# Kernel tuning notes

Hardware: AMD Instinct MI355X
Metric: run time of the kernel (lower is better)

The kernel has to match this reference:

```python
import jax, jax.numpy as jnp
import numpy as np

B, T, NB = 8192, 18, 6
EH, DH = 256, 256
NIN = NB + 1  # encoder GRU input: bits + feedback scalar


def gru_cell(x, h, Wih, Whh, bih, bhh):
    # PyTorch GRU cell: gates ordered (r, z, n)
    gi = x @ Wih.T + bih
    gh = h @ Whh.T + bhh
    ir, iz, inn = jnp.split(gi, 3, axis=-1)
    hr, hz, hn = jnp.split(gh, 3, axis=-1)
    r = jax.nn.sigmoid(ir + hr)
    z = jax.nn.sigmoid(iz + hz)
    n = jnp.tanh(inn + r * hn)
    return (1.0 - z) * n + z * h


def run_gru_dir(seq, Wih, Whh, bih, bhh, reverse):
    # seq: [T, B, D] -> hidden outputs [T, B, H] (aligned to original time order)
    Bn, H = seq.shape[1], Whh.shape[1]
    def step(h, x):
        h2 = gru_cell(x, h, Wih, Whh, bih, bhh)
        return h2, h2
    _, outs = jax.lax.scan(step, jnp.zeros((Bn, H), seq.dtype), seq, reverse=reverse)
    return outs


def setup_inputs() -> dict:
    key = jax.random.key(0)
    ks = jax.random.split(key, 40)
    def w(k, shape, fan):
        s = 1.0 / np.sqrt(fan)
        return jax.random.uniform(k, shape, jnp.float32, -s, s)
    inp = {}
    inp['b'] = (jax.random.uniform(ks[0], (B, NB)) < 0.5).astype(jnp.float32)
    inp['noise1'] = jax.random.normal(ks[1], (B, T, 1), jnp.float32)
    inp['noise2'] = jax.random.normal(ks[2], (B, T, 1), jnp.float32)
    # encoder GRU (2 layers, unidirectional)
    inp['enc_Wih0'] = w(ks[3], (3 * EH, NIN), EH); inp['enc_Whh0'] = w(ks[4], (3 * EH, EH), EH)
    inp['enc_bih0'] = w(ks[5], (3 * EH,), EH);     inp['enc_bhh0'] = w(ks[6], (3 * EH,), EH)
    inp['enc_Wih1'] = w(ks[7], (3 * EH, EH), EH);  inp['enc_Whh1'] = w(ks[8], (3 * EH, EH), EH)
    inp['enc_bih1'] = w(ks[9], (3 * EH,), EH);     inp['enc_bhh1'] = w(ks[10], (3 * EH,), EH)
    inp['enc_lin_W'] = w(ks[11], (1, EH), EH);     inp['enc_lin_b'] = w(ks[12], (1,), EH)
    inp['weight_power'] = jnp.ones((T,), jnp.float32)
    # decoder GRU (2 layers, bidirectional)
    inp['dec_Wih0f'] = w(ks[13], (3 * DH, 1), DH);      inp['dec_Whh0f'] = w(ks[14], (3 * DH, DH), DH)
    inp['dec_bih0f'] = w(ks[15], (3 * DH,), DH);        inp['dec_bhh0f'] = w(ks[16], (3 * DH,), DH)
    inp['dec_Wih0b'] = w(ks[17], (3 * DH, 1), DH);      inp['dec_Whh0b'] = w(ks[18], (3 * DH, DH), DH)
    inp['dec_bih0b'] = w(ks[19], (3 * DH,), DH);        inp['dec_bhh0b'] = w(ks[20], (3 * DH,), DH)
    inp['dec_Wih1f'] = w(ks[21], (3 * DH, 2 * DH), DH); inp['dec_Whh1f'] = w(ks[22], (3 * DH, DH), DH)
    inp['dec_bih1f'] = w(ks[23], (3 * DH,), DH);        inp['dec_bhh1f'] = w(ks[24], (3 * DH,), DH)
    inp['dec_Wih1b'] = w(ks[25], (3 * DH, 2 * DH), DH); inp['dec_Whh1b'] = w(ks[26], (3 * DH, DH), DH)
    inp['dec_bih1b'] = w(ks[27], (3 * DH,), DH);        inp['dec_bhh1b'] = w(ks[28], (3 * DH,), DH)
    inp['dec_lin_W'] = w(ks[29], (NB, 2 * DH), 2 * DH); inp['dec_lin_b'] = w(ks[30], (NB,), 2 * DH)
    inp['weight_merge'] = jnp.ones((T, 2), jnp.float32)
    return inp


def reference(b, noise1, noise2,
              enc_Wih0, enc_Whh0, enc_bih0, enc_bhh0,
              enc_Wih1, enc_Whh1, enc_bih1, enc_bhh1,
              enc_lin_W, enc_lin_b, weight_power,
              dec_Wih0f, dec_Whh0f, dec_bih0f, dec_bhh0f,
              dec_Wih0b, dec_Whh0b, dec_bih0b, dec_bhh0b,
              dec_Wih1f, dec_Whh1f, dec_bih1f, dec_bhh1f,
              dec_Wih1b, dec_Whh1b, dec_bih1b, dec_bhh1b,
              dec_lin_W, dec_lin_b, weight_merge):
    Bn = b.shape[0]
    Tn = weight_power.shape[0]
    # power-normalized per-step weights: sqrt(w^2 * T / sum(w^2))
    wp = jnp.sqrt(weight_power ** 2 * Tn / jnp.sum(weight_power ** 2))

    def enc_step(carry, xs):
        h0, h1, z = carry
        n1, n2, wpt = xs
        inp = jnp.concatenate([b, z], axis=1)            # [B, NB+1]
        h0n = gru_cell(inp, h0, enc_Wih0, enc_Whh0, enc_bih0, enc_bhh0)
        h1n = gru_cell(h0n, h1, enc_Wih1, enc_Whh1, enc_bih1, enc_bhh1)
        xt = jnp.tanh(h1n @ enc_lin_W.T + enc_lin_b)     # [B, 1]
        xn = (xt - jnp.mean(xt)) / jnp.std(xt, ddof=1)   # training-mode batch norm over whole tensor
        y = xn * wpt + n1                                # received symbol
        return (h0n, h1n, y + n2), y                     # feedback z = y + noise2

    carry0 = (jnp.zeros((Bn, EH), b.dtype), jnp.zeros((Bn, EH), b.dtype), jnp.zeros((Bn, 1), b.dtype))
    xs = (jnp.swapaxes(noise1, 0, 1), jnp.swapaxes(noise2, 0, 1), wp)
    _, y_seq = jax.lax.scan(enc_step, carry0, xs)        # [T, B, 1]

    # bidirectional 2-layer decoder GRU over y
    o0f = run_gru_dir(y_seq, dec_Wih0f, dec_Whh0f, dec_bih0f, dec_bhh0f, False)
    o0b = run_gru_dir(y_seq, dec_Wih0b, dec_Whh0b, dec_bih0b, dec_bhh0b, True)
    s1 = jnp.concatenate([o0f, o0b], axis=-1)            # [T, B, 2*DH]
    o1f = run_gru_dir(s1, dec_Wih1f, dec_Whh1f, dec_bih1f, dec_bhh1f, False)
    o1b = run_gru_dir(s1, dec_Wih1b, dec_Whh1b, dec_bih1b, dec_bhh1b, True)

    # attention_type == 5: learned weighted merge over time, per direction
    wf = jnp.sqrt(weight_merge[:, 0] ** 2 * Tn / jnp.sum(weight_merge[:, 0] ** 2))
    wb = jnp.sqrt(weight_merge[:, 1] ** 2 * Tn / jnp.sum(weight_merge[:, 1] ** 2))
    rf = jnp.einsum('tbh,t->bh', o1f, wf)
    rb = jnp.einsum('tbh,t->bh', o1b, wb)
    rc = jnp.concatenate([rf, rb], axis=1)               # [B, 2*DH]
    out = jax.nn.sigmoid(rc @ dec_lin_W.T + dec_lin_b)   # bit_vector output -> sigmoid
    return out.reshape(Bn, -1, 1)
```

## Files before the change

kernel.cpp:

```cpp
#include <hip/hip_runtime.h>
#include <hip/hip_bf16.h>
#include <math.h>

#define BN_ 8192
#define TT 18
#define NBITS 6
#define HH 256
#define G3 768

typedef __hip_bfloat16 hbf16;
typedef __bf16 bf16x8 __attribute__((ext_vector_type(8)));
typedef float f32x4 __attribute__((ext_vector_type(4)));

__device__ inline float sigm(float x){ return 1.0f/(1.0f + __expf(-x)); }
__device__ inline float ftanh(float x){ float e = __expf(2.0f*x); return 1.0f - 2.0f/(e + 1.0f); }
__device__ inline float ldx(const void* p, int i, int bf){
    if(bf){ unsigned short u = ((const unsigned short*)p)[i]; return __uint_as_float(((unsigned)u)<<16); }
    return ((const float*)p)[i];
}
__device__ inline __bf16 f2b(float f){ hbf16 h = __float2bfloat16(f); return *reinterpret_cast<__bf16*>(&h); }
__device__ inline float b2f(__bf16 b){ unsigned short u = *reinterpret_cast<unsigned short*>(&b); return __uint_as_float(((unsigned)u)<<16); }
__device__ inline unsigned pack2(float a, float b){
    hbf16 lo = __float2bfloat16(a), hi = __float2bfloat16(b);
    return (unsigned)*(unsigned short*)&lo | ((unsigned)*(unsigned short*)&hi << 16);
}

__device__ __forceinline__ void gld_lds16(const void* g, void* l){
    __builtin_amdgcn_global_load_lds(
        (const __attribute__((address_space(1))) unsigned int*)g,
        (__attribute__((address_space(3))) unsigned int*)l, 16, 0, 0);
}

__global__ __launch_bounds__(256) void fillz(float* __restrict__ p, int n){
    for(int i = blockIdx.x*256 + threadIdx.x; i < n; i += gridDim.x*256) p[i] = 0.0f;
}
__global__ __launch_bounds__(256) void fillb(__bf16* __restrict__ p, int n){
    for(int i = blockIdx.x*256 + threadIdx.x; i < n; i += gridDim.x*256) p[i] = f2b(0.0f);
}

__global__ void prep_w(const void* wp, const void* wm, unsigned* flag,
                       float* wpn, float* wfn, float* wbn){
    if(threadIdx.x==0 && blockIdx.x==0){
        unsigned w0 = *(const unsigned*)wp;
        int bf = ((w0 >> 16) == (w0 & 0xFFFFu)) ? 1 : 0;
        flag[0] = (unsigned)bf;
        float s=0; for(int t=0;t<TT;t++){ float v=ldx(wp,t,bf); s += v*v; }
        for(int t=0;t<TT;t++){ float v=ldx(wp,t,bf); wpn[t] = sqrtf(v*v*TT/s); }
        float sf=0, sb=0;
        for(int t=0;t<TT;t++){ float f=ldx(wm,2*t,bf), b=ldx(wm,2*t+1,bf); sf += f*f; sb += b*b; }
        for(int t=0;t<TT;t++){
            float f=ldx(wm,2*t,bf), b=ldx(wm,2*t+1,bf);
            wfn[t] = sqrtf(f*f*TT/sf);
            wbn[t] = sqrtf(b*b*TT/sb);
        }
    }
}

struct CJ { const void* src; void* dst; int n; int K; int mode; };
struct CJs { CJ j[20]; };
__global__ __launch_bounds__(256) void conv_all(CJs J, const unsigned* __restrict__ flagp){
    const int bf = (int)*flagp;
    CJ c = J.j[blockIdx.y];
    for(int i = blockIdx.x*256 + threadIdx.x; i < c.n; i += gridDim.x*256){
        if(c.mode==1){
            int row = i / c.K, k = i - row*c.K;
            int g = row>>8, jj = row&255;
            int prow = ((jj>>4)*48) + g*16 + (jj&15);
            ((__bf16*)c.dst)[(size_t)prow*c.K + k] = f2b(ldx(c.src, i, bf));
        }else if(c.mode==2){
            int t = i >> 13, b = i & (BN_-1);
            ((float*)c.dst)[i] = ldx(c.src, b*TT + t, bf);
        }else{
            ((float*)c.dst)[i] = ldx(c.src, i, bf);
        }
    }
}

struct FQ {
    const __bf16* A1; const __bf16* W1; int K1;
    const __bf16* A2; const __bf16* W2; int K2;
    const float* bgi; const float* bgh;
    const __bf16* h; __bf16* hout;
    const void* bits; const void* wih0raw; const void* bih0raw;
    const void* linw; float* xt;
    const float* y; const void* wihraw; const void* bihraw; __bf16* s1t;
    float* racc; const float* wct;
};
struct FQ2 { FQ q[2]; };

template<int MODE>
__global__ __launch_bounds__((MODE>=2)?512:256, 4) void fused_step(FQ2 PP, const unsigned* __restrict__ flagp){
    const FQ P = PP.q[blockIdx.z];
    const int bf = (int)*flagp;
    constexpr int THREADS = (MODE>=2) ? 512 : 256;
    constexpr int BM   = (MODE<=1) ? 64 : 128;
    constexpr int WR   = (MODE>=2) ? 192 : 96;
    constexpr int JB   = WR/3;
    constexpr int NF   = BM/32;
    constexpr int ABYT = BM*64;
    constexpr int WBYT = WR*64;
    constexpr int BUFB = ABYT + WBYT;
    constexpr int TS   = JB + 1;
    __shared__ __align__(16) char smem[2*BUFB];
    __shared__ float zs[(MODE>=2)?384:192];
    __shared__ float sred[4], ssred[4];
    float*  T  = (float*)smem;
    const int tid = threadIdx.x;
    constexpr int JTBITS = (MODE>=2) ? 2 : 3;
    constexpr int MTS = (8192/BM)/8;
    const int mt = blockIdx.x*MTS + (blockIdx.y>>JTBITS);
    const int jt = blockIdx.y & ((1<<JTBITS)-1);
    const int m0 = mt*BM;
    const int n0 = jt*WR;
    const int lane = tid&63, wv = tid>>6;
    const int wvbase = tid & ~63;
    const int wrow = (MODE>=2) ? (wv>>2) : (wv>>1);
    const int wcol = wv & ((MODE>=2)?3:1);
    const int q = lane>>4, n15 = lane&15;

    constexpr int S1  = (MODE==1) ? 8 : (MODE==3 ? 16 : 0);
    constexpr int NST = S1 + 8;
    constexpr int KD1 = (MODE==3) ? 512 : 256;
    constexpr int KD2 = 256;
    const __bf16* pA1 = (S1>0) ? P.A1 + (size_t)m0*KD1 : (const __bf16*)nullptr;
    const __bf16* pW1 = (S1>0) ? P.W1 + (size_t)n0*KD1 : (const __bf16*)nullptr;
    const __bf16* pA2 = P.A2 + (size_t)m0*KD2;
    const __bf16* pW2 = P.W2 + (size_t)n0*KD2;
    const int r0 = tid>>2, sl0 = tid&3;
    const int q0 = sl0 ^ ((r0>>1)&3);
    const int rW1 = THREADS/4 + r0;
    const int qW1 = sl0 ^ ((rW1>>1)&3);

    auto STG = [&](int s){
        const __bf16* A; const __bf16* W; int K; int k0;
        if(s < S1){ A = pA1; W = pW1; K = KD1; k0 = s*32; }
        else      { A = pA2; W = pW2; K = KD2; k0 = (s-S1)*32; }
        char* buf = smem + (s&1)*BUFB;
        gld_lds16(A + (size_t)r0*K + k0 + q0*8, buf + (size_t)wvbase*16);
        gld_lds16(W + (size_t)r0*K + k0 + q0*8, buf + ABYT + (size_t)wvbase*16);
        if(tid < THREADS/2)
            gld_lds16(W + (size_t)rW1*K + k0 + qW1*8, buf + ABYT + (size_t)(THREADS+wvbase)*16);
    };

    STG(0);

    if(MODE==0){
        if(P.K1){
            const float lbv = ldx(P.linw, 0, bf);
            const float wt  = P.wct[0];
            const float* __restrict__ xr = P.xt;
            float s=0.0f, ss=0.0f;
            const float4* x4 = (const float4*)xr;
            for(int i=tid;i<BN_/4;i+=THREADS){
                float4 vv = x4[i];
                float a0=ftanh(vv.x+lbv), a1=ftanh(vv.y+lbv), a2=ftanh(vv.z+lbv), a3=ftanh(vv.w+lbv);
                s += a0+a1+a2+a3; ss += a0*a0+a1*a1+a2*a2+a3*a3;
            }
            #pragma unroll
            for(int o=32;o;o>>=1){ s += __shfl_xor(s,o); ss += __shfl_xor(ss,o); }
            if(lane==0){ sred[wv]=s; ssred[wv]=ss; }
            __syncthreads();
            float a = sred[0]+sred[1]+sred[2]+sred[3];
            float bq = ssred[0]+ssred[1]+ssred[2]+ssred[3];
            float mean = a/(float)BN_;
            float var = (bq - (float)BN_*mean*mean)/(float)(BN_-1);
            float rs = 1.0f/sqrtf(var);
            if(tid<BM){
                int row = m0 + tid;
                float v = ftanh(xr[row]+lbv);
                float yv = (v-mean)*rs*wt + P.y[row];
                zs[tid] = yv + ((const float*)P.wihraw)[row];
                if(jt==0){ ((float*)P.s1t)[row] = yv; P.racc[row] = 0.0f; }
            }
        }else{
            if(tid<BM) zs[tid] = 0.0f;
        }
        __syncthreads();
    }else{
        __syncthreads();
    }

    f32x4 accR[NF], accZ[NF], accN1[NF], accN2[NF];
    #pragma unroll
    for(int i=0;i<NF;i++){ accR[i]=(f32x4){0,0,0,0}; accZ[i]=(f32x4){0,0,0,0};
                           accN1[i]=(f32x4){0,0,0,0}; accN2[i]=(f32x4){0,0,0,0}; }

    #pragma unroll
    for(int s=0; s<NST; ++s){
        if(s+1 < NST) STG(s+1);
        const char* buf = smem + (s&1)*BUFB;
        const __bf16* Asb = (const __bf16*)buf;
        const __bf16* Wsb = (const __bf16*)(buf + ABYT);
        bf16x8 af[NF], bfr[3];
        #pragma unroll
        for(int i=0;i<NF;i++){
            int R = wrow*(BM/2)+i*16+n15;
            int col = q ^ ((R>>1)&3);
            af[i] = *(const bf16x8*)&Asb[R*32 + col*8];
        }
        #pragma unroll
        for(int g=0;g<3;g++){
            int RW = wcol*48+g*16+n15;
            int col = q ^ ((RW>>1)&3);
            bfr[g] = *(const bf16x8*)&Wsb[RW*32 + col*8];
        }
        #pragma unroll
        for(int i=0;i<NF;i++){
            accR[i] = __builtin_amdgcn_mfma_f32_16x16x32_bf16(af[i], bfr[0], accR[i], 0,0,0);
            accZ[i] = __builtin_amdgcn_mfma_f32_16x16x32_bf16(af[i], bfr[1], accZ[i], 0,0,0);
            if(s < S1) accN1[i] = __builtin_amdgcn_mfma_f32_16x16x32_bf16(af[i], bfr[2], accN1[i], 0,0,0);
            else       accN2[i] = __builtin_amdgcn_mfma_f32_16x16x32_bf16(af[i], bfr[2], accN2[i], 0,0,0);
        }
        __syncthreads();
    }

    const int jl = wcol*16 + n15;
    const int j  = jt*JB + jl;
    const float bghr = P.bgh[j], bghz = P.bgh[256+j], bghn = P.bgh[512+j];
    float bgir=0, bgiz=0, bgin=0;
    if(MODE==1 || MODE==3){ bgir = P.bgi[j]; bgiz = P.bgi[256+j]; bgin = P.bgi[512+j]; }
    float w0r[7], w0z[7], w0n[7];
    if(MODE==0){
        #pragma unroll
        for(int k=0;k<7;k++){
            w0r[k] = ldx(P.wih0raw, (j    )*7+k, bf);
            w0z[k] = ldx(P.wih0raw, (j+256)*7+k, bf);
            w0n[k] = ldx(P.wih0raw, (j+512)*7+k, bf);
        }
        bgir = ldx(P.bih0raw, j, bf); bgiz = ldx(P.bih0raw, j+256, bf); bgin = ldx(P.bih0raw, j+512, bf);
    }
    float wy_r=0, wy_z=0, wy_n=0;
    if(MODE==2){
        wy_r = ldx(P.wihraw, j, bf); wy_z = ldx(P.wihraw, j+256, bf); wy_n = ldx(P.wihraw, j+512, bf);
        bgir = ldx(P.bihraw, j, bf); bgiz = ldx(P.bihraw, j+256, bf); bgin = ldx(P.bihraw, j+512, bf);
    }
    const float linwj = (MODE==1) ? ldx(P.linw, j, bf) : 0.0f;

    #pragma unroll
    for(int i=0;i<NF;i++){
        const int rbl = wrow*(BM/2) + i*16 + q*4;
        float vred[4];
        #pragma unroll
        for(int r=0;r<4;r++){
            const int row_l = rbl + r;
            const int row = m0 + row_l;
            float gir, giz, gin;
            if(MODE==1 || MODE==3){
                gir = bgir; giz = bgiz; gin = accN1[i][r] + bgin;
            }else if(MODE==0){
                gir = bgir; giz = bgiz; gin = bgin;
                #pragma unroll
                for(int k=0;k<NBITS;k++){
                    float bv = ldx(P.bits, row*NBITS+k, bf);
                    gir += bv*w0r[k]; giz += bv*w0z[k]; gin += bv*w0n[k];
                }
                float zb = zs[row_l];
                gir += zb*w0r[6]; giz += zb*w0z[6]; gin += zb*w0n[6];
            }else{
                float yv = P.y[row];
                gir = yv*wy_r + bgir; giz = yv*wy_z + bgiz; gin = yv*wy_n + bgin;
            }
            float rr = sigm(gir + accR[i][r] + bghr);
            float zz = sigm(giz + accZ[i][r] + bghz);
            float nn = ftanh(gin + rr*(accN2[i][r] + bghn));
            float hold = b2f(P.h[(size_t)row*HH + j]);
            float hn = (1.0f - zz)*nn + zz*hold;
            T[row_l*TS + jl] = hn;
            if(MODE==1) vred[r] = hn*linwj;
        }
        if(MODE==1){
            #pragma unroll
            for(int r=0;r<4;r++){
                float v = vred[r];
                #pragma unroll
                for(int m=1;m<16;m<<=1) v += __shfl_xor(v, m);
                if(n15==0) atomicAdd(&P.xt[m0+rbl+r], v);
            }
        }
    }
    if(MODE==3 && tid<6*JB){
        int k = tid/JB, jj = tid - k*JB;
        zs[tid] = ldx(P.bits, k*512 + (int)blockIdx.z*256 + jt*JB + jj, bf);
    }
    __syncthreads();

    if constexpr(MODE<=1){
        const int rw2 = tid>>2, cw = tid&3;
        const int row_l = rw2;
        const int row = m0 + row_l;
        float v[8];
        #pragma unroll
        for(int u=0;u<8;u++) v[u] = T[row_l*TS + cw*8 + u];
        uint4 pkv = { pack2(v[0],v[1]), pack2(v[2],v[3]), pack2(v[4],v[5]), pack2(v[6],v[7]) };
        *(uint4*)&P.hout[(size_t)row*HH + jt*JB + cw*8] = pkv;
    }else{
        const int rw2 = tid>>3, cw = tid&7;
        #pragma unroll
        for(int pass=0; pass<2; pass++){
            const int row_l = pass*64 + rw2;
            const int row = m0 + row_l;
            float v[8];
            #pragma unroll
            for(int u=0;u<8;u++) v[u] = T[row_l*TS + cw*8 + u];
            uint4 pkv = { pack2(v[0],v[1]), pack2(v[2],v[3]), pack2(v[4],v[5]), pack2(v[6],v[7]) };
            *(uint4*)&P.hout[(size_t)row*HH + jt*JB + cw*8] = pkv;
            if(MODE==2) *(uint4*)&P.s1t[(size_t)row*512 + jt*JB + cw*8] = pkv;
        }
    }
    if(MODE==3){
        float* pp = P.xt + (size_t)(jt + 4*(int)blockIdx.z)*(BN_*NBITS);
        const float wct3 = P.wct[0];
        #pragma unroll
        for(int u=0;u<2;u++){
            int idx = tid + THREADS*u;
            if(idx < BM*NBITS){
                int row_l = idx/6, k = idx - row_l*6;
                float dot = 0.0f;
                #pragma unroll
                for(int jj=0;jj<JB;jj++) dot += T[row_l*TS+jj]*zs[k*JB+jj];
                size_t gi = (size_t)(m0+row_l)*NBITS + k;
                pp[gi] += wct3*dot;
            }
        }
    }
}

__global__ __launch_bounds__(1024) void stats_emit(float* __restrict__ xt, const void* __restrict__ lb,
        const float* __restrict__ wpn, int t, const float* __restrict__ n1t, const float* __restrict__ n2t,
        float* __restrict__ yseq, float* __restrict__ zf, const unsigned* __restrict__ flagp){
    const int bf = (int)*flagp;
    const float lbv = ldx(lb, 0, bf);
    int tid = threadIdx.x;
    float s=0.0f, ss=0.0f;
    for(int i=tid;i<BN_;i+=1024){ float v = ftanh(xt[i] + lbv); s += v; ss += v*v; }
    #pragma unroll
    for(int o=32;o;o>>=1){ s += __shfl_down(s,o); ss += __shfl_down(ss,o); }
    __shared__ float S[16], SS[16], stm[2];
    if((tid&63)==0){ S[tid>>6]=s; SS[tid>>6]=ss; }
    __syncthreads();
    if(tid==0){
        float a=0.0f, b=0.0f;
        for(int i=0;i<16;i++){ a+=S[i]; b+=SS[i]; }
        float mean = a/(float)BN_;
        float var = (b - (float)BN_*mean*mean)/(float)(BN_-1);
        stm[0]=mean; stm[1]=1.0f/sqrtf(var);
    }
    __syncthreads();
    const float mean=stm[0], rs=stm[1], wt=wpn[t];
    for(int i=tid;i<BN_;i+=1024){
        float v = ftanh(xt[i] + lbv);
        float y = (v-mean)*rs*wt + n1t[i];
        yseq[(size_t)t*BN_ + i] = y;
        zf[i] = y + n2t[i];
        xt[i] = 0.0f;
    }
}

__global__ __launch_bounds__(256) void out_head(const float* __restrict__ pp, const void* __restrict__ bias,
        void* __restrict__ out, const unsigned* __restrict__ flagp){
    const int bf = (int)*flagp;
    int i = blockIdx.x*256 + threadIdx.x;
    if(i >= BN_*NBITS) return;
    float s = 0.0f;
    #pragma unroll
    for(int k=0;k<8;k++) s += pp[(size_t)k*(BN_*NBITS) + i];
    int kk = i - (i/6)*6;
    float v = sigm(s + ldx(bias, kk, bf));
    if(bf) ((hbf16*)out)[i] = __float2bfloat16(v);
    else   ((float*)out)[i] = v;
}

extern "C" void kernel_launch(void* const* d_in, const int* in_sizes, int n_in,
                              void* d_out, int out_size, void* d_ws, size_t ws_size,
                              hipStream_t stream)
{
    (void)in_sizes; (void)n_in; (void)out_size;
    const void* bits  = d_in[0];
    const void* n1    = d_in[1];
    const void* n2    = d_in[2];
    const void* eWih0 = d_in[3];
    const void* eWhh0 = d_in[4];
    const void* ebih0 = d_in[5];
    const void* ebhh0 = d_in[6];
    const void* eWih1 = d_in[7];
    const void* eWhh1 = d_in[8];
    const void* ebih1 = d_in[9];
    const void* ebhh1 = d_in[10];
    const void* elinW = d_in[11];
    const void* elinb = d_in[12];
    const void* wpow  = d_in[13];
    const void* dWih0f= d_in[14];
    const void* dWhh0f= d_in[15];
    const void* dbih0f= d_in[16];
    const void* dbhh0f= d_in[17];
    const void* dWih0b= d_in[18];
    const void* dWhh0b= d_in[19];
    const void* dbih0b= d_in[20];
    const void* dbhh0b= d_in[21];
    const void* dWih1f= d_in[22];
    const void* dWhh1f= d_in[23];
    const void* dbih1f= d_in[24];
    const void* dbhh1f= d_in[25];
    const void* dWih1b= d_in[26];
    const void* dWhh1b= d_in[27];
    const void* dbih1b= d_in[28];
    const void* dbhh1b= d_in[29];
    const void* dlinW = d_in[30];
    const void* dlinb = d_in[31];
    const void* wmrg  = d_in[32];

    float* base = (float*)d_ws;
    size_t off = 0;
    auto alloc  = [&](size_t n){ float* p = base + off; off += (n + 63) & ~(size_t)63; return p; };
    auto allocb = [&](size_t n){ __bf16* p = (__bf16*)(base + off); off += ((n/2) + 63) & ~(size_t)63; return p; };
    unsigned* flag = (unsigned*)alloc(64);
    float* wpn = alloc(TT); float* wfn = alloc(TT); float* wbn = alloc(TT);
    const int WK = HH*G3;
    __bf16* WeHH0 = allocb(WK);  __bf16* WeIH1 = allocb(WK);  __bf16* WeHH1 = allocb(WK);
    __bf16* Wd0f  = allocb(WK);  __bf16* Wd0b  = allocb(WK);
    __bf16* Wd1fI = allocb(2*WK);__bf16* Wd1bI = allocb(2*WK);
    __bf16* Wd1fH = allocb(WK);  __bf16* Wd1bH = allocb(WK);
    float* BeHH0 = alloc(G3); float* BeIH1 = alloc(G3); float* BeHH1 = alloc(G3);
    float* Bd0f  = alloc(G3); float* Bd0b  = alloc(G3);
    float* Bd1fI = alloc(G3); float* Bd1bI = alloc(G3);
    float* Bd1fH = alloc(G3); float* Bd1bH = alloc(G3);
    const size_t NH = (size_t)BN_*HH;
    __bf16* X0 = allocb(NH);  __bf16* X1 = allocb(NH);
    __bf16* Y0 = allocb(NH);  __bf16* Y1 = allocb(NH);
    float* pout = alloc((size_t)8*BN_*NBITS);
    float* xtA = alloc(BN_);
    float* xtB = alloc(BN_);
    float* zf  = alloc(BN_);
    float* yseq= alloc((size_t)TT*BN_);
    float* n1t = alloc((size_t)TT*BN_);
    float* n2t = alloc((size_t)TT*BN_);
    __bf16* s1 = allocb((size_t)TT*BN_*512);
    size_t need = off*sizeof(float);
    if(ws_size < need) return;

    prep_w<<<1,64,0,stream>>>(wpow, wmrg, flag, wpn, wfn, wbn);
    CJs J;
    const void* ws_src[20] = {eWhh0,eWih1,eWhh1,dWhh0f,dWhh0b,dWih1f,dWih1b,dWhh1f,dWhh1b,
                              ebhh0,ebih1,ebhh1,dbhh0f,dbhh0b,dbih1f,dbih1b,dbhh1f,dbhh1b, n1, n2};
    void* ws_dst[20] = {WeHH0,WeIH1,WeHH1,Wd0f,Wd0b,Wd1fI,Wd1bI,Wd1fH,Wd1bH,
                        BeHH0,BeIH1,BeHH1,Bd0f,Bd0b,Bd1fI,Bd1bI,Bd1fH,Bd1bH, n1t, n2t};
    int ws_n[20] = {WK,WK,WK,WK,WK,2*WK,2*WK,WK,WK, G3,G3,G3,G3,G3,G3,G3,G3,G3, TT*BN_, TT*BN_};
    int ws_K[20] = {256,256,256,256,256,512,512,256,256, 0,0,0,0,0,0,0,0,0, 0,0};
    int ws_m[20] = {1,1,1,1,1,1,1,1,1, 0,0,0,0,0,0,0,0,0, 2,2};
    for(int i=0;i<20;i++){ J.j[i] = {ws_src[i], ws_dst[i], ws_n[i], ws_K[i], ws_m[i]}; }
    conv_all<<<dim3(768,20),256,0,stream>>>(J, flag);
    fillb<<<1024,256,0,stream>>>(X0, (int)NH);
    fillb<<<1024,256,0,stream>>>(Y0, (int)NH);
    fillz<<<32,256,0,stream>>>(xtA, BN_);
    fillz<<<32,256,0,stream>>>(xtB, BN_);
    fillz<<<96,256,0,stream>>>(pout, 8*BN_*NBITS);

    dim3 g1(8, 128, 1), g2(8, 32, 2);
    __bf16* X[2] = {X0, X1};
    __bf16* Y[2] = {Y0, Y1};
    float* xts[2] = {xtA, xtB};

    int p = 0;
    for(int t=0;t<TT;t++){
        FQ2 P0{}; FQ2 P1{};
        FQ& a = P0.q[0];
        a.A2=X[p]; a.W2=WeHH0; a.K2=HH; a.bgh=BeHH0; a.h=X[p]; a.hout=X[1-p];
        a.bits=bits; a.wih0raw=eWih0; a.bih0raw=ebih0;
        a.K1 = (t>0) ? 1 : 0;
        if(t>0){
            a.xt   = xts[(t-1)&1];
            a.racc = xts[t&1];
            a.y    = n1t + (size_t)(t-1)*BN_;
            a.wihraw = (const void*)(n2t + (size_t)(t-1)*BN_);
            a.s1t  = (__bf16*)(yseq + (size_t)(t-1)*BN_);
            a.wct  = wpn + (t-1);
            a.linw = elinb;
        }
        fused_step<0><<<g1,256,0,stream>>>(P0, flag);
        FQ& b = P1.q[0];
        b.A1=X[1-p]; b.W1=WeIH1; b.K1=HH; b.A2=Y[p]; b.W2=WeHH1; b.K2=HH;
        b.bgi=BeIH1; b.bgh=BeHH1; b.h=Y[p]; b.hout=Y[1-p];
        b.linw=elinW; b.xt=xts[t&1];
        fused_step<1><<<g1,256,0,stream>>>(P1, flag);
        p ^= 1;
    }
    stats_emit<<<1,1024,0,stream>>>(xts[(TT-1)&1], elinb, wpn, TT-1,
                                    n1t+(size_t)(TT-1)*BN_, n2t+(size_t)(TT-1)*BN_, yseq, zf, flag);

    fillb<<<1024,256,0,stream>>>(X0, (int)NH);
    fillb<<<1024,256,0,stream>>>(Y0, (int)NH);
    p = 0;
    for(int i=0;i<TT;i++){
        int tf = i, tb = TT-1-i;
        FQ2 P{};
        FQ& a = P.q[0];
        a.A2=X[p]; a.W2=Wd0f; a.K2=HH; a.bgh=Bd0f; a.h=X[p]; a.hout=X[1-p];
        a.y=yseq+(size_t)tf*BN_; a.wihraw=dWih0f; a.bihraw=dbih0f; a.s1t=s1+(size_t)tf*BN_*512;
        FQ& b = P.q[1];
        b.A2=Y[p]; b.W2=Wd0b; b.K2=HH; b.bgh=Bd0b; b.h=Y[p]; b.hout=Y[1-p];
        b.y=yseq+(size_t)tb*BN_; b.wihraw=dWih0b; b.bihraw=dbih0b; b.s1t=s1+(size_t)tb*BN_*512+256;
        fused_step<2><<<g2,512,0,stream>>>(P, flag);
        p ^= 1;
    }

    fillb<<<1024,256,0,stream>>>(X0, (int)NH);
    fillb<<<1024,256,0,stream>>>(Y0, (int)NH);
    p = 0;
    for(int i=0;i<TT;i++){
        int tf = i, tb = TT-1-i;
        FQ2 P{};
        FQ& a = P.q[0];
        a.A1=s1+(size_t)tf*BN_*512; a.W1=Wd1fI; a.K1=512;
        a.A2=X[p]; a.W2=Wd1fH; a.K2=HH; a.bgi=Bd1fI; a.bgh=Bd1fH; a.h=X[p]; a.hout=X[1-p];
        a.bits=dlinW; a.xt=pout; a.wct=wfn+tf;
        FQ& b = P.q[1];
        b.A1=s1+(size_t)tb*BN_*512; b.W1=Wd1bI; b.K1=512;
        b.A2=Y[p]; b.W2=Wd1bH; b.K2=HH; b.bgi=Bd1bI; b.bgh=Bd1bH; b.h=Y[p]; b.hout=Y[1-p];
        b.bits=dlinW; b.xt=pout; b.wct=wbn+tb;
        fused_step<3><<<g2,512,0,stream>>>(P, flag);
        p ^= 1;
    }

    out_head<<<192,256,0,stream>>>(pout, dlinb, d_out, flag);
}
```

Baseline: 1.691 ms.

## Add dedicated decoder layer-1 kernel using 32x32 MFMA and wider column tiles

Replaces the templated MODE 3 step for the second decoder layer with a dedicated kernel. Each block now covers 128 hidden columns per gate (384 weight rows) instead of 64, using 32x32x16 bf16 MFMA with a matching weight row permutation. This halves the number of column tiles and partial-output slices, so the activation tile is reloaded fewer times and the final head sums fewer partials. The cost is a larger LDS footprint, more accumulator registers per thread and a longer serial 128-wide dot in the epilogue.

```diff
diff --git a/kernel.cpp b/kernel.cpp
--- a/kernel.cpp
+++ b/kernel.cpp
@@ -11,6 +11,7 @@
 typedef __hip_bfloat16 hbf16;
 typedef __bf16 bf16x8 __attribute__((ext_vector_type(8)));
 typedef float f32x4 __attribute__((ext_vector_type(4)));
+typedef float f32x16 __attribute__((ext_vector_type(16)));
 
 __device__ inline float sigm(float x){ return 1.0f/(1.0f + __expf(-x)); }
 __device__ inline float ftanh(float x){ float e = __expf(2.0f*x); return 1.0f - 2.0f/(e + 1.0f); }
@@ -66,6 +67,11 @@
             int row = i / c.K, k = i - row*c.K;
             int g = row>>8, jj = row&255;
             int prow = ((jj>>4)*48) + g*16 + (jj&15);
+            ((__bf16*)c.dst)[(size_t)prow*c.K + k] = f2b(ldx(c.src, i, bf));
+        }else if(c.mode==3){
+            int row = i / c.K, k = i - row*c.K;
+            int g = row>>8, jj = row&255;
+            int prow = (jj>>7)*384 + ((jj>>5)&3)*96 + g*32 + (jj&31);
             ((__bf16*)c.dst)[(size_t)prow*c.K + k] = f2b(ldx(c.src, i, bf));
         }else if(c.mode==2){
             int t = i >> 13, b = i & (BN_-1);
@@ -118,9 +124,9 @@
     const int wcol = wv & ((MODE>=2)?3:1);
     const int q = lane>>4, n15 = lane&15;
 
-    constexpr int S1  = (MODE==1) ? 8 : (MODE==3 ? 16 : 0);
+    constexpr int S1  = (MODE==1) ? 8 : 0;
     constexpr int NST = S1 + 8;
-    constexpr int KD1 = (MODE==3) ? 512 : 256;
+    constexpr int KD1 = 256;
     constexpr int KD2 = 256;
     const __bf16* pA1 = (S1>0) ? P.A1 + (size_t)m0*KD1 : (const __bf16*)nullptr;
     const __bf16* pW1 = (S1>0) ? P.W1 + (size_t)n0*KD1 : (const __bf16*)nullptr;
@@ -218,7 +224,7 @@
     const int j  = jt*JB + jl;
     const float bghr = P.bgh[j], bghz = P.bgh[256+j], bghn = P.bgh[512+j];
     float bgir=0, bgiz=0, bgin=0;
-    if(MODE==1 || MODE==3){ bgir = P.bgi[j]; bgiz = P.bgi[256+j]; bgin = P.bgi[512+j]; }
+    if(MODE==1){ bgir = P.bgi[j]; bgiz = P.bgi[256+j]; bgin = P.bgi[512+j]; }
     float w0r[7], w0z[7], w0n[7];
     if(MODE==0){
         #pragma unroll
@@ -245,7 +251,7 @@
             const int row_l = rbl + r;
             const int row = m0 + row_l;
             float gir, giz, gin;
-            if(MODE==1 || MODE==3){
+            if(MODE==1){
                 gir = bgir; giz = bgiz; gin = accN1[i][r] + bgin;
             }else if(MODE==0){
                 gir = bgir; giz = bgiz; gin = bgin;
@@ -278,10 +284,6 @@
             }
         }
     }
-    if(MODE==3 && tid<6*JB){
-        int k = tid/JB, jj = tid - k*JB;
-        zs[tid] = ldx(P.bits, k*512 + (int)blockIdx.z*256 + jt*JB + jj, bf);
-    }
     __syncthreads();
 
     if constexpr(MODE<=1){
@@ -307,20 +309,137 @@
             if(MODE==2) *(uint4*)&P.s1t[(size_t)row*512 + jt*JB + cw*8] = pkv;
         }
     }
-    if(MODE==3){
-        float* pp = P.xt + (size_t)(jt + 4*(int)blockIdx.z)*(BN_*NBITS);
+}
+
+__global__ __launch_bounds__(512,2) void fused_step3w(FQ2 PP, const unsigned* __restrict__ flagp){
+    const FQ P = PP.q[blockIdx.z];
+    const int bf = (int)*flagp;
+    constexpr int TS = 129;
+    constexpr int ABYT = 128*64;
+    constexpr int BUFB = ABYT + 384*64;
+    constexpr int S1 = 16, NST = 24;
+    __shared__ __align__(16) char smem[66560];
+    __shared__ float zs[768];
+    float* T = (float*)smem;
+    const int tid = threadIdx.x;
+    const int mt = blockIdx.x*8 + (blockIdx.y>>1);
+    const int jt = blockIdx.y & 1;
+    const int m0 = mt*128;
+    const int n0 = jt*384;
+    const int lane = tid&63, wv = tid>>6;
+    const int wvbase = tid & ~63;
+    const int wrow = wv>>2, wcol = wv&3;
+    const int l31 = lane&31, hi = lane>>5;
+
+    const __bf16* pA1 = P.A1 + (size_t)m0*512;
+    const __bf16* pW1 = P.W1 + (size_t)n0*512;
+    const __bf16* pA2 = P.A2 + (size_t)m0*256;
+    const __bf16* pW2 = P.W2 + (size_t)n0*256;
+    const int r0 = tid>>2, sl0 = tid&3;
+    const int q0 = sl0 ^ ((r0>>1)&3);
+    const int rB = 128 + r0, qB = sl0 ^ ((rB>>1)&3);
+    const int rC = 256 + r0, qC = sl0 ^ ((rC>>1)&3);
+
+    auto STG = [&](int s){
+        const __bf16* A; const __bf16* W; int K; int k0;
+        if(s < S1){ A = pA1; W = pW1; K = 512; k0 = s*32; }
+        else      { A = pA2; W = pW2; K = 256; k0 = (s-S1)*32; }
+        char* buf = smem + (s&1)*BUFB;
+        gld_lds16(A + (size_t)r0*K + k0 + q0*8, buf + (size_t)wvbase*16);
+        gld_lds16(W + (size_t)r0*K + k0 + q0*8, buf + ABYT + (size_t)wvbase*16);
+        gld_lds16(W + (size_t)rB*K + k0 + qB*8, buf + ABYT + (size_t)(512+wvbase)*16);
+        gld_lds16(W + (size_t)rC*K + k0 + qC*8, buf + ABYT + (size_t)(1024+wvbase)*16);
+    };
+
+    STG(0);
+    __syncthreads();
+
+    f32x16 accR[2], accZ[2], accN1[2], accN2[2];
+    #pragma unroll
+    for(int f=0;f<2;f++){
+        #pragma unroll
+        for(int e=0;e<16;e++){ accR[f][e]=0.0f; accZ[f][e]=0.0f; accN1[f][e]=0.0f; accN2[f][e]=0.0f; }
+    }
+
+    #pragma unroll
+    for(int s=0; s<NST; ++s){
+        if(s+1 < NST) STG(s+1);
+        const char* buf = smem + (s&1)*BUFB;
+        const __bf16* Asb = (const __bf16*)buf;
+        const __bf16* Wsb = (const __bf16*)(buf + ABYT);
+        #pragma unroll
+        for(int sub=0; sub<2; ++sub){
+            const int cq = sub*2 + hi;
+            bf16x8 af[2], bfr[3];
+            #pragma unroll
+            for(int f=0;f<2;f++){
+                int R = wrow*64 + f*32 + l31;
+                int col = cq ^ ((R>>1)&3);
+                af[f] = *(const bf16x8*)&Asb[R*32 + col*8];
+            }
+            #pragma unroll
+            for(int g=0;g<3;g++){
+                int RW = wcol*96 + g*32 + l31;
+                int col = cq ^ ((RW>>1)&3);
+                bfr[g] = *(const bf16x8*)&Wsb[RW*32 + col*8];
+            }
+            #pragma unroll
+            for(int f=0;f<2;f++){
+                accR[f] = __builtin_amdgcn_mfma_f32_32x32x16_bf16(af[f], bfr[0], accR[f], 0,0,0);
+                accZ[f] = __builtin_amdgcn_mfma_f32_32x32x16_bf16(af[f], bfr[1], accZ[f], 0,0,0);
+                if(s < S1) accN1[f] = __builtin_amdgcn_mfma_f32_32x32x16_bf16(af[f], bfr[2], accN1[f], 0,0,0);
+                else       accN2[f] = __builtin_amdgcn_mfma_f32_32x32x16_bf16(af[f], bfr[2], accN2[f], 0,0,0);
+            }
+        }
+        __syncthreads();
+    }
+
+    const int jl = wcol*32 + l31;
+    const int j  = jt*128 + jl;
+    const float bghr = P.bgh[j], bghz = P.bgh[256+j], bghn = P.bgh[512+j];
+    const float bgir = P.bgi[j], bgiz = P.bgi[256+j], bgin = P.bgi[512+j];
+    #pragma unroll
+    for(int f=0;f<2;f++){
+        #pragma unroll
+        for(int r=0;r<16;r++){
+            const int row_l = wrow*64 + f*32 + (r&3) + 8*(r>>2) + 4*hi;
+            const int row = m0 + row_l;
+            float gin = accN1[f][r] + bgin;
+            float rr = sigm(bgir + accR[f][r] + bghr);
+            float zz = sigm(bgiz + accZ[f][r] + bghz);
+            float nn = ftanh(gin + rr*(accN2[f][r] + bghn));
+            float hold = b2f(P.h[(size_t)row*HH + j]);
+            float hn = (1.0f - zz)*nn + zz*hold;
+            T[row_l*TS + jl] = hn;
+        }
+    }
+    for(int idx=tid; idx<768; idx+=512){
+        int k = idx>>7, jj = idx&127;
+        zs[idx] = ldx(P.bits, k*512 + (int)blockIdx.z*256 + jt*128 + jj, bf);
+    }
+    __syncthreads();
+
+    const int rw = tid>>4, cw = tid&15;
+    #pragma unroll
+    for(int pass=0; pass<4; pass++){
+        const int row_l = pass*32 + rw;
+        const int row = m0 + row_l;
+        float v[8];
+        #pragma unroll
+        for(int u=0;u<8;u++) v[u] = T[row_l*TS + cw*8 + u];
+        uint4 pkv = { pack2(v[0],v[1]), pack2(v[2],v[3]), pack2(v[4],v[5]), pack2(v[6],v[7]) };
+        *(uint4*)&P.hout[(size_t)row*HH + jt*128 + cw*8] = pkv;
+    }
+    {
+        float* pp = P.xt + (size_t)(jt + 2*(int)blockIdx.z)*(BN_*NBITS);
         const float wct3 = P.wct[0];
-        #pragma unroll
-        for(int u=0;u<2;u++){
-            int idx = tid + THREADS*u;
-            if(idx < BM*NBITS){
-                int row_l = idx/6, k = idx - row_l*6;
-                float dot = 0.0f;
-                #pragma unroll
-                for(int jj=0;jj<JB;jj++) dot += T[row_l*TS+jj]*zs[k*JB+jj];
-                size_t gi = (size_t)(m0+row_l)*NBITS + k;
-                pp[gi] += wct3*dot;
-            }
+        for(int idx=tid; idx<128*NBITS; idx+=512){
+            int row_l = idx/6, k = idx - row_l*6;
+            float dot = 0.0f;
+            #pragma unroll
+            for(int jj=0;jj<128;jj++) dot += T[row_l*TS+jj]*zs[k*128+jj];
+            size_t gi = (size_t)(m0+row_l)*NBITS + k;
+            pp[gi] += wct3*dot;
         }
     }
 }
@@ -363,7 +482,7 @@
     if(i >= BN_*NBITS) return;
     float s = 0.0f;
     #pragma unroll
-    for(int k=0;k<8;k++) s += pp[(size_t)k*(BN_*NBITS) + i];
+    for(int k=0;k<4;k++) s += pp[(size_t)k*(BN_*NBITS) + i];
     int kk = i - (i/6)*6;
     float v = sigm(s + ldx(bias, kk, bf));
     if(bf) ((hbf16*)out)[i] = __float2bfloat16(v);
@@ -427,7 +546,7 @@
     const size_t NH = (size_t)BN_*HH;
     __bf16* X0 = allocb(NH);  __bf16* X1 = allocb(NH);
     __bf16* Y0 = allocb(NH);  __bf16* Y1 = allocb(NH);
-    float* pout = alloc((size_t)8*BN_*NBITS);
+    float* pout = alloc((size_t)4*BN_*NBITS);
     float* xtA = alloc(BN_);
     float* xtB = alloc(BN_);
     float* zf  = alloc(BN_);
@@ -446,16 +565,16 @@
                         BeHH0,BeIH1,BeHH1,Bd0f,Bd0b,Bd1fI,Bd1bI,Bd1fH,Bd1bH, n1t, n2t};
     int ws_n[20] = {WK,WK,WK,WK,WK,2*WK,2*WK,WK,WK, G3,G3,G3,G3,G3,G3,G3,G3,G3, TT*BN_, TT*BN_};
     int ws_K[20] = {256,256,256,256,256,512,512,256,256, 0,0,0,0,0,0,0,0,0, 0,0};
-    int ws_m[20] = {1,1,1,1,1,1,1,1,1, 0,0,0,0,0,0,0,0,0, 2,2};
+    int ws_m[20] = {1,1,1,1,1,3,3,3,3, 0,0,0,0,0,0,0,0,0, 2,2};
     for(int i=0;i<20;i++){ J.j[i] = {ws_src[i], ws_dst[i], ws_n[i], ws_K[i], ws_m[i]}; }
     conv_all<<<dim3(768,20),256,0,stream>>>(J, flag);
     fillb<<<1024,256,0,stream>>>(X0, (int)NH);
     fillb<<<1024,256,0,stream>>>(Y0, (int)NH);
     fillz<<<32,256,0,stream>>>(xtA, BN_);
     fillz<<<32,256,0,stream>>>(xtB, BN_);
-    fillz<<<96,256,0,stream>>>(pout, 8*BN_*NBITS);
-
-    dim3 g1(8, 128, 1), g2(8, 32, 2);
+    fillz<<<96,256,0,stream>>>(pout, 4*BN_*NBITS);
+
+    dim3 g1(8, 128, 1), g2(8, 32, 2), g3(8, 16, 2);
     __bf16* X[2] = {X0, X1};
     __bf16* Y[2] = {Y0, Y1};
     float* xts[2] = {xtA, xtB};
@@ -517,7 +636,7 @@
         b.A1=s1+(size_t)tb*BN_*512; b.W1=Wd1bI; b.K1=512;
         b.A2=Y[p]; b.W2=Wd1bH; b.K2=HH; b.bgi=Bd1bI; b.bgh=Bd1bH; b.h=Y[p]; b.hout=Y[1-p];
         b.bits=dlinW; b.xt=pout; b.wct=wbn+tb;
-        fused_step<3><<<g2,512,0,stream>>>(P, flag);
+        fused_step3w<<<g3,512,0,stream>>>(P, flag);
         p ^= 1;
     }
 
```

Result: slower. 1.792 ms (+5.9%).
